# Kernel optimization log

Measured on AMD Instinct MI355X. Metric: run time of the kernel, lower is better.

Reference implementation:

```python
import jax, jax.numpy as jnp
import numpy as np

D = 1024
H = 16
HD = D // H
DFF = 4 * D
EPS = 1e-12


def setup_inputs() -> dict:
    key = jax.random.key(0)
    ks = jax.random.split(key, 16)
    s = lambda fan_in: 1.0 / np.sqrt(fan_in)
    inp = {
        "x": jax.random.normal(ks[0], (2, 2048, D), dtype=jnp.float32),
        "Wq": jax.random.normal(ks[1], (D, D), dtype=jnp.float32) * s(D),
        "bq": jax.random.normal(ks[2], (D,), dtype=jnp.float32) * 0.02,
        "Wk": jax.random.normal(ks[3], (D, D), dtype=jnp.float32) * s(D),
        "bk": jax.random.normal(ks[4], (D,), dtype=jnp.float32) * 0.02,
        "Wv": jax.random.normal(ks[5], (D, D), dtype=jnp.float32) * s(D),
        "bv": jax.random.normal(ks[6], (D,), dtype=jnp.float32) * 0.02,
        "Wo": jax.random.normal(ks[7], (D, D), dtype=jnp.float32) * s(D),
        "bo": jax.random.normal(ks[8], (D,), dtype=jnp.float32) * 0.02,
        "W1": jax.random.normal(ks[9], (D, DFF), dtype=jnp.float32) * s(D),
        "b1": jax.random.normal(ks[10], (DFF,), dtype=jnp.float32) * 0.02,
        "W2": jax.random.normal(ks[11], (DFF, D), dtype=jnp.float32) * s(DFF),
        "b2": jax.random.normal(ks[12], (D,), dtype=jnp.float32) * 0.02,
        "g1": jnp.ones((D,), dtype=jnp.float32),
        "s1": jnp.zeros((D,), dtype=jnp.float32),
        "g2": jnp.ones((D,), dtype=jnp.float32),
        "s2": jnp.zeros((D,), dtype=jnp.float32),
    }
    return inp


def _layer_norm(x, scale, shift):
    mean = jnp.mean(x, axis=-1, keepdims=True)
    # torch.var default is unbiased (ddof=1), matching the source module
    var = jnp.var(x, axis=-1, keepdims=True, ddof=1)
    return scale * (x - mean) / jnp.sqrt(var + EPS) + shift


def _gelu(x):
    c = jnp.sqrt(jnp.asarray(2.0 / np.pi, dtype=x.dtype))
    return 0.5 * x * (1.0 + jnp.tanh(c * (x + 0.044715 * x ** 3)))


def _block(x, Wq, bq, Wk, bk, Wv, bv, Wo, bo, W1, b1, W2, b2, g1, s1, g2, s2):
    B, S, _ = x.shape
    # pre-norm attention
    h = _layer_norm(x, g1, s1)
    q = (h @ Wq + bq).reshape(B, S, H, HD).transpose(0, 2, 1, 3)  # bhsd
    k = (h @ Wk + bk).reshape(B, S, H, HD).transpose(0, 2, 1, 3)
    v = (h @ Wv + bv).reshape(B, S, H, HD).transpose(0, 2, 1, 3)
    scores = jnp.einsum("bhqd,bhkd->bhqk", q, k)
    causal = jnp.tril(jnp.ones((S, S), dtype=bool))  # True = keep
    scores = jnp.where(causal, scores, -jnp.inf)
    attn = jax.nn.softmax(scores / np.sqrt(HD), axis=-1)
    ctx = jnp.einsum("bhqk,bhkd->bhqd", attn, v)
    ctx = ctx.transpose(0, 2, 1, 3).reshape(B, S, D)
    x = x + (ctx @ Wo + bo)
    # pre-norm MLP
    h = _layer_norm(x, g2, s2)
    h = _gelu(h @ W1 + b1) @ W2 + b2
    return x + h


def reference(x, Wq, bq, Wk, bk, Wv, bv, Wo, bo, W1, b1, W2, b2, g1, s1, g2, s2):
    return _block(x, Wq, bq, Wk, bk, Wv, bv, Wo, bo, W1, b1, W2, b2, g1, s1, g2, s2)
```

## Files before the change

kernel.cpp:

```cpp
#include <hip/hip_runtime.h>

#define D_ 1024
#define H_ 16
#define HD_ 64
#define DFF_ 4096
#define B_ 2
#define S_ 2048
#define MTOK 4096

typedef unsigned short u16;
typedef short bf16x8 __attribute__((ext_vector_type(8)));
typedef float f32x4 __attribute__((ext_vector_type(4)));

__device__ __forceinline__ u16 f2bf(float f) {
    union { float f; unsigned u; } v; v.f = f;
    return (u16)((v.u + 0x7fffu + ((v.u >> 16) & 1u)) >> 16);
}
__device__ __forceinline__ u16 f2bf_ru(float f) {
    union { float f; unsigned u; } v; v.f = f;
    return (u16)((v.u + 0x8000u) >> 16);
}

__device__ __forceinline__ void gload16(const void* g, void* l) {
    __builtin_amdgcn_global_load_lds(
        (const __attribute__((address_space(1))) unsigned int*)g,
        (__attribute__((address_space(3))) unsigned int*)l, 16, 0, 0);
}

__global__ __launch_bounds__(256) void transpose_all_kernel(
    const float* __restrict__ Wq, const float* __restrict__ Wk,
    const float* __restrict__ Wv, const float* __restrict__ Wo,
    const float* __restrict__ W1, const float* __restrict__ W2,
    u16* __restrict__ bQKV, u16* __restrict__ bWo,
    u16* __restrict__ bW1, u16* __restrict__ bW2) {
    int b = blockIdx.x;
    const float* W; u16* Wt; int K, N, nt, kt;
    if (b < 4096) {
        int w = b >> 10, t = b & 1023;
        K = 1024; N = 1024; nt = t & 31; kt = t >> 5;
        W = (w == 0) ? Wq : (w == 1) ? Wk : (w == 2) ? Wv : Wo;
        Wt = (w < 3) ? (bQKV + (size_t)w * 1048576u) : bWo;
    } else if (b < 8192) {
        int t = b - 4096;
        K = 1024; N = 4096; nt = t & 127; kt = t >> 7;
        W = W1; Wt = bW1;
    } else {
        int t = b - 8192;
        K = 4096; N = 1024; nt = t & 31; kt = t >> 5;
        W = W2; Wt = bW2;
    }
    __shared__ float tl[32][33];
    int n0 = nt * 32, k0 = kt * 32;
    int tx = threadIdx.x, ty = threadIdx.y;
#pragma unroll
    for (int i = 0; i < 4; i++)
        tl[ty + i * 8][tx] = W[(size_t)(k0 + ty + i * 8) * N + n0 + tx];
    __syncthreads();
#pragma unroll
    for (int i = 0; i < 4; i++)
        Wt[(size_t)(n0 + ty + i * 8) * K + k0 + tx] = f2bf(tl[tx][ty + i * 8]);
}

__global__ __launch_bounds__(256) void ln_kernel(
    const float* __restrict__ x, const float* __restrict__ gamma,
    const float* __restrict__ beta, u16* __restrict__ out) {
    int row = blockIdx.x, tid = threadIdx.x;
    int wave = tid >> 6, lane = tid & 63;
    const float4* xr = (const float4*)(x + (size_t)row * D_);
    float4 v = xr[tid];
    float s = v.x + v.y + v.z + v.w;
#pragma unroll
    for (int off = 1; off < 64; off <<= 1) s += __shfl_xor(s, off, 64);
    __shared__ float p1[4], p2[4];
    if (lane == 0) p1[wave] = s;
    __syncthreads();
    float mean = (p1[0] + p1[1] + p1[2] + p1[3]) * (1.0f / D_);
    float4 d = {v.x - mean, v.y - mean, v.z - mean, v.w - mean};
    float sq = d.x * d.x + d.y * d.y + d.z * d.z + d.w * d.w;
#pragma unroll
    for (int off = 1; off < 64; off <<= 1) sq += __shfl_xor(sq, off, 64);
    if (lane == 0) p2[wave] = sq;
    __syncthreads();
    float var = (p2[0] + p2[1] + p2[2] + p2[3]) * (1.0f / (D_ - 1));
    float rstd = rsqrtf(var + 1e-12f);
    float4 gv = ((const float4*)gamma)[tid];
    float4 bv = ((const float4*)beta)[tid];
    u16* orow = out + (size_t)row * D_ + tid * 4;
    orow[0] = f2bf(gv.x * d.x * rstd + bv.x);
    orow[1] = f2bf(gv.y * d.y * rstd + bv.y);
    orow[2] = f2bf(gv.z * d.z * rstd + bv.z);
    orow[3] = f2bf(gv.w * d.w * rstd + bv.w);
}

constexpr int EPI_QKV = 0, EPI_O = 3, EPI_G = 4, EPI_R = 5;

template <int EPI, int KD, int TM, int BK, int GYB>
__global__ __launch_bounds__(256) void gemm_kernel(
    const u16* __restrict__ A, const u16* __restrict__ Bt,
    const float* __restrict__ bias, const float* __restrict__ bias2,
    const float* __restrict__ bias3, const float* __restrict__ resid,
    void* __restrict__ Cout) {
    __shared__ alignas(16) char Alds[3][TM * BK * 2];
    __shared__ alignas(16) char Blds[3][128 * BK * 2];
    int tid = threadIdx.x;
    int tm = (blockIdx.x & ((1 << GYB) - 1)) * TM;
    int tn = (blockIdx.x >> GYB) * 128;
    int wave = tid >> 6, lane = tid & 63;
    int wrow = (wave >> 1) * (TM / 2), wcol = (wave & 1) * 64;
    int lcol = lane & 15, quad = lane >> 4;
    constexpr int NI = TM / 32;
    constexpr int G = (BK == 32) ? 4 : 6;
    f32x4 acc[NI][4] = {};

    const u16 *ga, *gb;
    if constexpr (BK == 32) {
        int l = lane >> 3, p = lane & 7, slog = p ^ l;
        int sro = l * 2 + (slog >> 2), sch = slog & 3;
        ga = A + (size_t)(tm + wave * 16 + sro) * KD + sch * 8;
        gb = Bt + (size_t)(tn + wave * 16 + sro) * KD + sch * 8;
    } else {
        int g = (lane & 7) ^ (lane >> 3);
        ga = A + (size_t)(tm + wave * 16 + (lane >> 3)) * KD + g * 8;
        gb = Bt + (size_t)(tn + wave * 32 + (lane >> 3)) * KD + g * 8;
    }

    auto stage = [&](int k0, int slot) {
        if constexpr (BK == 32) {
            char* lA = Alds[slot] + wave * 1024;
            char* lB = Blds[slot] + wave * 1024;
            gload16(ga + k0, lA);
            gload16(ga + (size_t)64 * KD + k0, lA + 4096);
            gload16(gb + k0, lB);
            gload16(gb + (size_t)64 * KD + k0, lB + 4096);
        } else {
            char* lA = Alds[slot] + wave * 2048;
            gload16(ga + k0, lA);
            gload16(ga + (size_t)8 * KD + k0, lA + 1024);
            char* lB = Blds[slot] + wave * 4096;
            gload16(gb + k0, lB);
            gload16(gb + (size_t)8 * KD + k0, lB + 1024);
            gload16(gb + (size_t)16 * KD + k0, lB + 2048);
            gload16(gb + (size_t)24 * KD + k0, lB + 3072);
        }
    };

    constexpr int NT = KD / BK;
    stage(0, 0);
    stage(BK, 1);
#pragma unroll 1
    for (int kt = 0; kt < NT; kt++) {
        if (kt == NT - 1) {
            asm volatile("s_waitcnt vmcnt(0)" ::: "memory");
        } else if constexpr (G == 4) {
            asm volatile("s_waitcnt vmcnt(4)" ::: "memory");
        } else {
            asm volatile("s_waitcnt vmcnt(6)" ::: "memory");
        }
        asm volatile("s_barrier" ::: "memory");
        if (kt + 2 < NT) stage((kt + 2) * BK, (kt + 2) % 3);
        int cur = kt % 3;
        if constexpr (BK == 32) {
            int swz = (lcol >> 1) * 128 + (((((lcol & 1) << 2) | quad) ^ (lcol >> 1)) * 16);
            bf16x8 af[NI], bfr[4];
#pragma unroll
            for (int i = 0; i < NI; i++)
                af[i] = *(const bf16x8*)(Alds[cur] + wrow * 64 + i * 1024 + swz);
#pragma unroll
            for (int j = 0; j < 4; j++)
                bfr[j] = *(const bf16x8*)(Blds[cur] + wcol * 64 + j * 1024 + swz);
#pragma unroll
            for (int i = 0; i < NI; i++)
#pragma unroll
                for (int j = 0; j < 4; j++)
                    acc[i][j] = __builtin_amdgcn_mfma_f32_16x16x32_bf16(
                        af[i], bfr[j], acc[i][j], 0, 0, 0);
        } else {
            int koff0 = lcol * 128 + ((quad ^ (lcol & 7)) * 16);
            int koff1 = lcol * 128 + (((4 | quad) ^ (lcol & 7)) * 16);
            bf16x8 af0[NI], af1[NI], bf0[4], bf1[4];
#pragma unroll
            for (int i = 0; i < NI; i++) {
                af0[i] = *(const bf16x8*)(Alds[cur] + (wrow + i * 16) * 128 + koff0);
                af1[i] = *(const bf16x8*)(Alds[cur] + (wrow + i * 16) * 128 + koff1);
            }
#pragma unroll
            for (int j = 0; j < 4; j++) {
                bf0[j] = *(const bf16x8*)(Blds[cur] + (wcol + j * 16) * 128 + koff0);
                bf1[j] = *(const bf16x8*)(Blds[cur] + (wcol + j * 16) * 128 + koff1);
            }
#pragma unroll
            for (int i = 0; i < NI; i++)
#pragma unroll
                for (int j = 0; j < 4; j++)
                    acc[i][j] = __builtin_amdgcn_mfma_f32_16x16x32_bf16(
                        af0[i], bf0[j], acc[i][j], 0, 0, 0);
#pragma unroll
            for (int i = 0; i < NI; i++)
#pragma unroll
                for (int j = 0; j < 4; j++)
                    acc[i][j] = __builtin_amdgcn_mfma_f32_16x16x32_bf16(
                        af1[i], bf1[j], acc[i][j], 0, 0, 0);
        }
    }
#pragma unroll
    for (int i = 0; i < NI; i++)
#pragma unroll
        for (int j = 0; j < 4; j++)
#pragma unroll
            for (int r = 0; r < 4; r++) {
                int m = tm + wrow + i * 16 + quad * 4 + r;
                int n = tn + wcol + j * 16 + lcol;
                if constexpr (EPI == EPI_QKV) {
                    int which = n >> 10, d = n & 1023;
                    const float* bp = (which == 0) ? bias : (which == 1) ? bias2 : bias3;
                    float cval = acc[i][j][r] + bp[d];
                    int b = m >> 11, s = m & 2047, h = d >> 6, hd = d & 63;
                    u16* qkv = (u16*)Cout;
                    if (which == 0)
                        qkv[((size_t)(b * H_ + h) * S_ + s) * HD_ + hd] = f2bf(cval);
                    else if (which == 1)
                        qkv[4194304u + ((size_t)(b * H_ + h) * S_ + s) * HD_ + hd] = f2bf(cval);
                    else
                        qkv[8388608u + ((size_t)(b * H_ + h) * HD_ + hd) * S_ + s] = f2bf(cval);
                } else if constexpr (EPI == EPI_O) {
                    float cval = acc[i][j][r] + bias[n];
                    ((float*)Cout)[(size_t)m * D_ + n] = resid[(size_t)m * D_ + n] + cval;
                } else if constexpr (EPI == EPI_G) {
                    float cval = acc[i][j][r] + bias[n];
                    float u = 0.7978845608028654f * (cval + 0.044715f * cval * cval * cval);
                    float t = 1.0f - 2.0f / (__expf(2.0f * u) + 1.0f);
                    ((u16*)Cout)[(size_t)m * DFF_ + n] = f2bf(0.5f * cval * (1.0f + t));
                } else {
                    float cval = acc[i][j][r] + bias[n];
                    ((float*)Cout)[(size_t)m * D_ + n] = resid[(size_t)m * D_ + n] + cval;
                }
            }
}

__global__ __launch_bounds__(256) void attn_kernel(
    const u16* __restrict__ q, const u16* __restrict__ k,
    const u16* __restrict__ v, u16* __restrict__ ctx) {
    __shared__ alignas(16) u16 klds[3][64 * 64];
    __shared__ alignas(16) u16 vlds[3][64 * 64];
    __shared__ alignas(16) u16 plds[4][16 * 64];
    int tid = threadIdx.x, wave = tid >> 6, lane = tid & 63;
    int quad = lane >> 4, lcol = lane & 15;
    int bh = blockIdx.x & 31, pairi = blockIdx.x >> 5;
    const u16* qbase = q + (size_t)bh * S_ * HD_;
    const u16* kbase = k + (size_t)bh * S_ * HD_;
    const u16* vbase = v + (size_t)bh * HD_ * S_;
    int g = (lane & 7) ^ (lane >> 3);
    int srow = wave * 16 + (lane >> 3);
    const u16* kp = kbase + (size_t)srow * HD_ + g * 8;
    const u16* vp = vbase + (size_t)srow * S_ + g * 8;
    char* pbase = (char*)plds + wave * 2048;
    int koff0 = lcol * 128 + ((quad ^ (lcol & 7)) * 16);
    int koff1 = lcol * 128 + (((4 | quad) ^ (lcol & 7)) * 16);
    int b = bh >> 4, h = bh & 15;
    auto stage = [&](int kt, int slot) {
        int k0 = kt * 64;
        char* kd = (char*)klds[slot] + wave * 2048;
        char* vd = (char*)vlds[slot] + wave * 2048;
        gload16(kp + (size_t)k0 * HD_, kd);
        gload16(kp + (size_t)(k0 + 8) * HD_, kd + 1024);
        gload16(vp + k0, vd);
        gload16(vp + 8 * S_ + k0, vd + 1024);
    };
#pragma unroll 1
    for (int half = 0; half < 2; half++) {
        int qt = half ? (31 - pairi) : pairi;
        int qr = qt * 64 + wave * 16;
        bf16x8 aq0 = *(const bf16x8*)(qbase + (size_t)(qr + lcol) * HD_ + quad * 8);
        bf16x8 aq1 = *(const bf16x8*)(qbase + (size_t)(qr + lcol) * HD_ + 32 + quad * 8);
        f32x4 co[4] = {};
        float li[4] = {0.0f, 0.0f, 0.0f, 0.0f};
        __syncthreads();
        stage(0, 0);
        if (qt >= 1) stage(1, 1);
#pragma unroll 1
        for (int kt = 0; kt <= qt; kt++) {
            if (kt == qt) {
                asm volatile("s_waitcnt vmcnt(0)" ::: "memory");
            } else {
                asm volatile("s_waitcnt vmcnt(4)" ::: "memory");
            }
            asm volatile("s_barrier" ::: "memory");
            if (kt + 2 <= qt) stage(kt + 2, (kt + 2) % 3);
            const u16* kl = klds[kt % 3];
            const u16* vl = vlds[kt % 3];
            f32x4 cs[4] = {};
#pragma unroll
            for (int j = 0; j < 4; j++) {
                bf16x8 bk = *(const bf16x8*)((char*)kl + j * 2048 + koff0);
                cs[j] = __builtin_amdgcn_mfma_f32_16x16x32_bf16(aq0, bk, cs[j], 0, 0, 0);
            }
#pragma unroll
            for (int j = 0; j < 4; j++) {
                bf16x8 bk = *(const bf16x8*)((char*)kl + j * 2048 + koff1);
                cs[j] = __builtin_amdgcn_mfma_f32_16x16x32_bf16(aq1, bk, cs[j], 0, 0, 0);
            }
            bool diag = (kt == qt);
#pragma unroll
            for (int r = 0; r < 4; r++) {
                int rr = quad * 4 + r;
                float p[4], ls = 0.0f;
#pragma unroll
                for (int j = 0; j < 4; j++) {
                    float sv = cs[j][r];
                    if (diag && (j * 16 + lcol > wave * 16 + rr)) sv = -1e38f;
                    p[j] = exp2f(sv * 0.18033688011112042f);
                    ls += p[j];
                }
                li[r] += ls;
                int pr = rr * 128 + (lcol & 7) * 2;
#pragma unroll
                for (int j = 0; j < 4; j++)
                    *(u16*)(pbase + pr + (((j * 2 + (lcol >> 3)) ^ (rr & 7)) * 16)) = f2bf_ru(p[j]);
            }
            {
                bf16x8 ap0 = *(const bf16x8*)(pbase + koff0);
                bf16x8 ap1 = *(const bf16x8*)(pbase + koff1);
#pragma unroll
                for (int j = 0; j < 4; j++) {
                    bf16x8 bv0 = *(const bf16x8*)((char*)vl + j * 2048 + koff0);
                    co[j] = __builtin_amdgcn_mfma_f32_16x16x32_bf16(ap0, bv0, co[j], 0, 0, 0);
                }
#pragma unroll
                for (int j = 0; j < 4; j++) {
                    bf16x8 bv1 = *(const bf16x8*)((char*)vl + j * 2048 + koff1);
                    co[j] = __builtin_amdgcn_mfma_f32_16x16x32_bf16(ap1, bv1, co[j], 0, 0, 0);
                }
            }
        }
#pragma unroll
        for (int r = 0; r < 4; r++) {
            float l = li[r];
            l += __shfl_xor(l, 1);
            l += __shfl_xor(l, 2);
            l += __shfl_xor(l, 4);
            l += __shfl_xor(l, 8);
            float inv = 1.0f / l;
            int row = qr + quad * 4 + r;
            size_t base = ((size_t)(b * S_ + row)) * D_ + h * HD_;
#pragma unroll
            for (int j = 0; j < 4; j++)
                ctx[base + j * 16 + lcol] = f2bf(co[j][r] * inv);
        }
    }
}

extern "C" void kernel_launch(void* const* d_in, const int* in_sizes, int n_in,
                              void* d_out, int out_size, void* d_ws, size_t ws_size,
                              hipStream_t stream) {
    const float* x  = (const float*)d_in[0];
    const float* Wq = (const float*)d_in[1];
    const float* bq = (const float*)d_in[2];
    const float* Wk = (const float*)d_in[3];
    const float* bk = (const float*)d_in[4];
    const float* Wv = (const float*)d_in[5];
    const float* bv = (const float*)d_in[6];
    const float* Wo = (const float*)d_in[7];
    const float* bo = (const float*)d_in[8];
    const float* W1 = (const float*)d_in[9];
    const float* b1 = (const float*)d_in[10];
    const float* W2 = (const float*)d_in[11];
    const float* b2 = (const float*)d_in[12];
    const float* g1 = (const float*)d_in[13];
    const float* s1 = (const float*)d_in[14];
    const float* g2 = (const float*)d_in[15];
    const float* s2 = (const float*)d_in[16];

    char* ws = (char*)d_ws;
    const size_t MB = 1024 * 1024;
    u16*   bWqkv = (u16*)(ws + 0 * MB);
    u16*   bWo   = (u16*)(ws + 6 * MB);
    u16*   bW1   = (u16*)(ws + 8 * MB);
    u16*   bW2   = (u16*)(ws + 16 * MB);
    u16*   hbuf  = (u16*)(ws + 24 * MB);
    u16*   qbuf  = (u16*)(ws + 32 * MB);
    u16*   ctxb  = (u16*)(ws + 56 * MB);
    float* x1    = (float*)(ws + 64 * MB);
    u16*   ffb   = (u16*)(ws + 80 * MB);

    transpose_all_kernel<<<12288, dim3(32, 8), 0, stream>>>(
        Wq, Wk, Wv, Wo, W1, W2, bWqkv, bWo, bW1, bW2);

    ln_kernel<<<MTOK, 256, 0, stream>>>(x, g1, s1, hbuf);

    gemm_kernel<EPI_QKV, D_, 128, 32, 5><<<768, 256, 0, stream>>>(
        hbuf, bWqkv, bq, bk, bv, nullptr, qbuf);

    attn_kernel<<<512, 256, 0, stream>>>(
        qbuf, qbuf + 4194304u, qbuf + 8388608u, ctxb);

    gemm_kernel<EPI_O, D_, 64, 64, 6><<<512, 256, 0, stream>>>(
        ctxb, bWo, bo, nullptr, nullptr, x, x1);

    ln_kernel<<<MTOK, 256, 0, stream>>>(x1, g2, s2, hbuf);

    gemm_kernel<EPI_G, D_, 128, 32, 5><<<1024, 256, 0, stream>>>(
        hbuf, bW1, b1, nullptr, nullptr, nullptr, ffb);

    gemm_kernel<EPI_R, DFF_, 64, 64, 6><<<512, 256, 0, stream>>>(
        ffb, bW2, b2, nullptr, nullptr, x1, (float*)d_out);
}
```

Baseline: 354.3 us.

## Add 256x128-tile GEMM kernel for QKV and FFN-up projections

Introduces a larger-tile GEMM (256x128 per block, each wave owning 64 rows and all 128 columns) with a 3-stage LDS pipeline and swizzled loads. It is used for the QKV and W1 GEMMs, halving block counts, and the epilogue is factored into a shared helper. The goal is higher arithmetic intensity per LDS load and fewer redundant global loads. The cost is 128 accumulator registers per thread and fewer blocks than CUs for QKV (384), which may hurt occupancy and load balance.

```diff
diff --git a/kernel.cpp b/kernel.cpp
--- a/kernel.cpp
+++ b/kernel.cpp
@@ -94,6 +94,107 @@
 
 constexpr int EPI_QKV = 0, EPI_O = 3, EPI_G = 4, EPI_R = 5;
 
+template <int EPI>
+__device__ __forceinline__ void epi_store(
+    float accv, int m, int n, const float* bias, const float* bias2,
+    const float* bias3, const float* resid, void* Cout) {
+    if constexpr (EPI == EPI_QKV) {
+        int which = n >> 10, d = n & 1023;
+        const float* bp = (which == 0) ? bias : (which == 1) ? bias2 : bias3;
+        float cval = accv + bp[d];
+        int b = m >> 11, s = m & 2047, h = d >> 6, hd = d & 63;
+        u16* qkv = (u16*)Cout;
+        if (which == 0)
+            qkv[((size_t)(b * H_ + h) * S_ + s) * HD_ + hd] = f2bf(cval);
+        else if (which == 1)
+            qkv[4194304u + ((size_t)(b * H_ + h) * S_ + s) * HD_ + hd] = f2bf(cval);
+        else
+            qkv[8388608u + ((size_t)(b * H_ + h) * HD_ + hd) * S_ + s] = f2bf(cval);
+    } else if constexpr (EPI == EPI_O) {
+        float cval = accv + bias[n];
+        ((float*)Cout)[(size_t)m * D_ + n] = resid[(size_t)m * D_ + n] + cval;
+    } else if constexpr (EPI == EPI_G) {
+        float cval = accv + bias[n];
+        float u = 0.7978845608028654f * (cval + 0.044715f * cval * cval * cval);
+        float t = 1.0f - 2.0f / (__expf(2.0f * u) + 1.0f);
+        ((u16*)Cout)[(size_t)m * DFF_ + n] = f2bf(0.5f * cval * (1.0f + t));
+    } else {
+        float cval = accv + bias[n];
+        ((float*)Cout)[(size_t)m * D_ + n] = resid[(size_t)m * D_ + n] + cval;
+    }
+}
+
+template <int EPI, int KD, int GYB>
+__global__ __launch_bounds__(256, 2) void gemm_fat_kernel(
+    const u16* __restrict__ A, const u16* __restrict__ Bt,
+    const float* __restrict__ bias, const float* __restrict__ bias2,
+    const float* __restrict__ bias3, const float* __restrict__ resid,
+    void* __restrict__ Cout) {
+    __shared__ alignas(16) char Alds[3][16384];
+    __shared__ alignas(16) char Blds[3][8192];
+    int tid = threadIdx.x;
+    int tm = (blockIdx.x & ((1 << GYB) - 1)) * 256;
+    int tn = (blockIdx.x >> GYB) * 128;
+    int wave = tid >> 6, lane = tid & 63;
+    int lcol = lane & 15, quad = lane >> 4;
+    f32x4 acc[4][8] = {};
+
+    int l = lane >> 3, p = lane & 7, slog = p ^ l;
+    int sro = l * 2 + (slog >> 2), sch = slog & 3;
+    const u16* ga = A + (size_t)(tm + wave * 64 + sro) * KD + sch * 8;
+    const u16* gb = Bt + (size_t)(tn + wave * 32 + sro) * KD + sch * 8;
+
+    auto stage = [&](int k0, int slot) {
+        char* lA = Alds[slot] + wave * 4096;
+        char* lB = Blds[slot] + wave * 2048;
+        gload16(ga + k0, lA);
+        gload16(ga + (size_t)16 * KD + k0, lA + 1024);
+        gload16(ga + (size_t)32 * KD + k0, lA + 2048);
+        gload16(ga + (size_t)48 * KD + k0, lA + 3072);
+        gload16(gb + k0, lB);
+        gload16(gb + (size_t)16 * KD + k0, lB + 1024);
+    };
+
+    constexpr int NT = KD / 32;
+    stage(0, 0);
+    stage(32, 1);
+    int swz = (lcol >> 1) * 128 + (((((lcol & 1) << 2) | quad) ^ (lcol >> 1)) * 16);
+#pragma unroll 1
+    for (int kt = 0; kt < NT; kt++) {
+        if (kt == NT - 1) {
+            asm volatile("s_waitcnt vmcnt(0)" ::: "memory");
+        } else {
+            asm volatile("s_waitcnt vmcnt(6)" ::: "memory");
+        }
+        asm volatile("s_barrier" ::: "memory");
+        if (kt + 2 < NT) stage((kt + 2) * 32, (kt + 2) % 3);
+        int cur = kt % 3;
+        bf16x8 af[4], bfr[8];
+#pragma unroll
+        for (int i = 0; i < 4; i++)
+            af[i] = *(const bf16x8*)(Alds[cur] + wave * 4096 + i * 1024 + swz);
+#pragma unroll
+        for (int j = 0; j < 8; j++)
+            bfr[j] = *(const bf16x8*)(Blds[cur] + j * 1024 + swz);
+#pragma unroll
+        for (int i = 0; i < 4; i++)
+#pragma unroll
+            for (int j = 0; j < 8; j++)
+                acc[i][j] = __builtin_amdgcn_mfma_f32_16x16x32_bf16(
+                    af[i], bfr[j], acc[i][j], 0, 0, 0);
+    }
+#pragma unroll
+    for (int i = 0; i < 4; i++)
+#pragma unroll
+        for (int j = 0; j < 8; j++)
+#pragma unroll
+            for (int r = 0; r < 4; r++) {
+                int m = tm + wave * 64 + i * 16 + quad * 4 + r;
+                int n = tn + j * 16 + lcol;
+                epi_store<EPI>(acc[i][j][r], m, n, bias, bias2, bias3, resid, Cout);
+            }
+}
+
 template <int EPI, int KD, int TM, int BK, int GYB>
 __global__ __launch_bounds__(256) void gemm_kernel(
     const u16* __restrict__ A, const u16* __restrict__ Bt,
@@ -210,30 +311,7 @@
             for (int r = 0; r < 4; r++) {
                 int m = tm + wrow + i * 16 + quad * 4 + r;
                 int n = tn + wcol + j * 16 + lcol;
-                if constexpr (EPI == EPI_QKV) {
-                    int which = n >> 10, d = n & 1023;
-                    const float* bp = (which == 0) ? bias : (which == 1) ? bias2 : bias3;
-                    float cval = acc[i][j][r] + bp[d];
-                    int b = m >> 11, s = m & 2047, h = d >> 6, hd = d & 63;
-                    u16* qkv = (u16*)Cout;
-                    if (which == 0)
-                        qkv[((size_t)(b * H_ + h) * S_ + s) * HD_ + hd] = f2bf(cval);
-                    else if (which == 1)
-                        qkv[4194304u + ((size_t)(b * H_ + h) * S_ + s) * HD_ + hd] = f2bf(cval);
-                    else
-                        qkv[8388608u + ((size_t)(b * H_ + h) * HD_ + hd) * S_ + s] = f2bf(cval);
-                } else if constexpr (EPI == EPI_O) {
-                    float cval = acc[i][j][r] + bias[n];
-                    ((float*)Cout)[(size_t)m * D_ + n] = resid[(size_t)m * D_ + n] + cval;
-                } else if constexpr (EPI == EPI_G) {
-                    float cval = acc[i][j][r] + bias[n];
-                    float u = 0.7978845608028654f * (cval + 0.044715f * cval * cval * cval);
-                    float t = 1.0f - 2.0f / (__expf(2.0f * u) + 1.0f);
-                    ((u16*)Cout)[(size_t)m * DFF_ + n] = f2bf(0.5f * cval * (1.0f + t));
-                } else {
-                    float cval = acc[i][j][r] + bias[n];
-                    ((float*)Cout)[(size_t)m * D_ + n] = resid[(size_t)m * D_ + n] + cval;
-                }
+                epi_store<EPI>(acc[i][j][r], m, n, bias, bias2, bias3, resid, Cout);
             }
 }
 
@@ -387,7 +465,7 @@
 
     ln_kernel<<<MTOK, 256, 0, stream>>>(x, g1, s1, hbuf);
 
-    gemm_kernel<EPI_QKV, D_, 128, 32, 5><<<768, 256, 0, stream>>>(
+    gemm_fat_kernel<EPI_QKV, D_, 4><<<384, 256, 0, stream>>>(
         hbuf, bWqkv, bq, bk, bv, nullptr, qbuf);
 
     attn_kernel<<<512, 256, 0, stream>>>(
@@ -398,7 +476,7 @@
 
     ln_kernel<<<MTOK, 256, 0, stream>>>(x1, g2, s2, hbuf);
 
-    gemm_kernel<EPI_G, D_, 128, 32, 5><<<1024, 256, 0, stream>>>(
+    gemm_fat_kernel<EPI_G, D_, 4><<<512, 256, 0, stream>>>(
         hbuf, bW1, b1, nullptr, nullptr, nullptr, ffb);
 
     gemm_kernel<EPI_R, DFF_, 64, 64, 6><<<512, 256, 0, stream>>>(
```

Result: slower. 367.7 us (+3.8%).
